# Kernel optimization log

Hardware: AMD Instinct MI355X
Metric: run time of the kernel (lower is better)

Reference implementation:

```python
import jax, jax.numpy as jnp
import numpy as np

B, C, H, W = 4096, 1, 64, 64
NCLASS = 10
ALPHA = 1.0
EPS = 1e-8  # torch CosineSimilarity eps


def setup_inputs() -> dict:
    key = jax.random.key(0)
    k1, k2, k3 = jax.random.split(key, 3)
    outputs = jax.random.normal(k1, (B, NCLASS), dtype=jnp.float32)
    grad = jax.random.normal(k2, (B, C, H, W), dtype=jnp.float32)
    y = jax.random.randint(k3, (B,), 0, NCLASS)
    return {"outputs": outputs, "grad": grad, "y": y}


def reference(outputs, grad, y):
    b = grad.shape[0]
    # per-sample min-max normalization over all of (C,H,W)
    flat = grad.reshape(b, -1)                      # [B, C*H*W]
    gmax = flat.max(axis=1, keepdims=True)
    gmin = flat.min(axis=1, keepdims=True)
    ngrad = (flat - gmin) / (gmax - gmin)           # [B, D]

    # batched pairwise cosine similarity: normalize + matmul
    norms = jnp.linalg.norm(ngrad, axis=1, keepdims=True)
    vn = ngrad / jnp.maximum(norms, EPS)
    sim = vn @ vn.T                                 # [B, B]

    # pairs (i<j) with the same predicted class (argmax(softmax(o)) == argmax(o))
    pred = jnp.argmax(outputs, axis=1)
    same = pred[:, None] == pred[None, :]
    upper = jnp.triu(jnp.ones((b, b), dtype=bool), k=1)
    mask = same & upper
    xloss = jnp.sum(jnp.where(mask, 1.0 - sim, 0.0)) / b

    # cross-entropy
    logp = jax.nn.log_softmax(outputs, axis=1)
    celoss = -jnp.take_along_axis(logp, y[:, None], axis=1).sum() / b
    return celoss + ALPHA * xloss
```

## Files before the change

kernel.cpp:

```cpp
#include <hip/hip_runtime.h>
#include <math.h>

constexpr int Dn = 4096;
constexpr int Bn = 4096;
constexpr int NCLS = 10;
constexpr int CH = 4;
constexpr int MAXCH = Bn / CH + NCLS;

constexpr int OFF_CUR  = 0;
constexpr int OFF_CE   = 10;
constexpr int OFF_XS   = 11;
constexpr int OFF_DONE = 12;
constexpr int OFF_ORD  = 16;
constexpr int OFF_P    = 41024;

__global__ __launch_bounds__(256) void pass0_ce_order(
    const float* __restrict__ outputs, const int* __restrict__ y,
    float* __restrict__ ws)
{
    const int t = threadIdx.x;
    const int i = blockIdx.x * 256 + t;
    const int w = t >> 6, lane = t & 63;
    int* wsi = (int*)ws;

    __shared__ int hist[NCLS];
    __shared__ int lbase[NCLS];
    __shared__ float sce[4];
    if (t < NCLS) hist[t] = 0;
    __syncthreads();

    const float* o = outputs + (size_t)i * NCLS;
    float m = o[0]; int am = 0;
    #pragma unroll
    for (int k = 1; k < NCLS; ++k) { float ok = o[k]; if (ok > m) { m = ok; am = k; } }
    float se = 0.f;
    #pragma unroll
    for (int k = 0; k < NCLS; ++k) se += expf(o[k] - m);
    float ce = m + logf(se) - o[y[i]];

    int rank = atomicAdd(&hist[am], 1);

    #pragma unroll
    for (int off = 32; off; off >>= 1) ce += __shfl_down(ce, off, 64);
    if (lane == 0) sce[w] = ce;
    __syncthreads();

    if (t < NCLS) lbase[t] = atomicAdd(&wsi[OFF_CUR + t], hist[t]);
    if (t == 0) atomicAdd(&ws[OFF_CE], sce[0] + sce[1] + sce[2] + sce[3]);
    __syncthreads();

    wsi[OFF_ORD + am * Bn + lbase[am] + rank] = i;
}

__global__ __launch_bounds__(256) void pass12_fused(
    const float* __restrict__ grad, float* __restrict__ ws)
{
    const int* wsi = (const int*)ws;
    const int t = threadIdx.x, w = t >> 6, lane = t & 63;

    int c = -1, s0 = 0, cnt = 0;
    {
        int b = (int)blockIdx.x, acc = 0;
        #pragma unroll
        for (int k = 0; k < NCLS; ++k) {
            int n = wsi[OFF_CUR + k];
            int nch = (n + CH - 1) / CH;
            if (c < 0 && b < acc + nch) { c = k; s0 = (b - acc) * CH; cnt = n; }
            acc += nch;
        }
    }
    if (c < 0) return;
    const int m = min(CH, cnt - s0);

    float4 v[16];
    if (w < m) {
        const int idx = wsi[OFF_ORD + c * Bn + s0 + w];
        const float4* row = (const float4*)grad + (size_t)idx * (Dn / 4);
        #pragma unroll
        for (int k = 0; k < 16; ++k) v[k] = row[k * 64 + lane];

        float mn = fminf(fminf(v[0].x, v[0].y), fminf(v[0].z, v[0].w));
        #pragma unroll
        for (int k = 1; k < 16; ++k)
            mn = fminf(mn, fminf(fminf(v[k].x, v[k].y), fminf(v[k].z, v[k].w)));
        #pragma unroll
        for (int off = 1; off < 64; off <<= 1)
            mn = fminf(mn, __shfl_xor(mn, off, 64));

        float ss = 0.f;
        #pragma unroll
        for (int k = 0; k < 16; ++k) {
            float dx = v[k].x - mn, dy = v[k].y - mn;
            float dz = v[k].z - mn, dw = v[k].w - mn;
            ss += dx * dx + dy * dy + dz * dz + dw * dw;
        }
        #pragma unroll
        for (int off = 1; off < 64; off <<= 1)
            ss += __shfl_xor(ss, off, 64);

        const float a = 1.0f / sqrtf(ss);
        const float b = -mn * a;
        #pragma unroll
        for (int k = 0; k < 16; ++k) {
            v[k].x = fmaf(v[k].x, a, b);
            v[k].y = fmaf(v[k].y, a, b);
            v[k].z = fmaf(v[k].z, a, b);
            v[k].w = fmaf(v[k].w, a, b);
        }
    } else {
        #pragma unroll
        for (int k = 0; k < 16; ++k) v[k] = make_float4(0.f, 0.f, 0.f, 0.f);
    }

    __shared__ float4 buf0[1024];
    __shared__ float4 buf1[1024];
    if (w == 2) {
        #pragma unroll
        for (int k = 0; k < 16; ++k) buf0[k * 64 + lane] = v[k];
    }
    if (w == 3) {
        #pragma unroll
        for (int k = 0; k < 16; ++k) buf1[k * 64 + lane] = v[k];
    }
    __syncthreads();
    if (w == 0) {
        #pragma unroll
        for (int k = 0; k < 16; ++k) {
            float4 u = buf0[k * 64 + lane];
            v[k].x += u.x; v[k].y += u.y; v[k].z += u.z; v[k].w += u.w;
        }
    }
    if (w == 1) {
        #pragma unroll
        for (int k = 0; k < 16; ++k) {
            float4 u = buf1[k * 64 + lane];
            v[k].x += u.x; v[k].y += u.y; v[k].z += u.z; v[k].w += u.w;
            buf1[k * 64 + lane] = v[k];
        }
    }
    __syncthreads();
    if (w == 0) {
        float4* Pc = (float4*)(ws + OFF_P) + (size_t)blockIdx.x * (Dn / 4);
        #pragma unroll
        for (int k = 0; k < 16; ++k) {
            float4 u = buf1[k * 64 + lane];
            v[k].x += u.x; v[k].y += u.y; v[k].z += u.z; v[k].w += u.w;
            Pc[k * 64 + lane] = v[k];
        }
    }
}

__global__ __launch_bounds__(256) void pass34_final(
    float* __restrict__ ws, float* __restrict__ out)
{
    const int t = threadIdx.x;
    const int idx = blockIdx.x * 256 + t;
    const int c = idx >> 12;
    const int j = idx & (Dn - 1);
    const int w = t >> 6, lane = t & 63;
    const int* wsi = (const int*)ws;

    int cs = 0, ce2 = 0;
    {
        int acc = 0;
        #pragma unroll
        for (int k = 0; k < NCLS; ++k) {
            int nch = (wsi[OFF_CUR + k] + CH - 1) / CH;
            if (k == c) { cs = acc; ce2 = acc + nch; }
            acc += nch;
        }
    }

    const float* P = ws + OFF_P;
    float s = 0.f;
    int ch = cs;
    for (; ch + 4 <= ce2; ch += 4)
        s += P[(size_t)(ch + 0) * Dn + j] + P[(size_t)(ch + 1) * Dn + j]
           + P[(size_t)(ch + 2) * Dn + j] + P[(size_t)(ch + 3) * Dn + j];
    for (; ch < ce2; ++ch) s += P[(size_t)ch * Dn + j];
    float p = s * s;

    #pragma unroll
    for (int off = 32; off; off >>= 1) p += __shfl_down(p, off, 64);
    __shared__ float sr[4];
    if (lane == 0) sr[w] = p;
    __syncthreads();
    if (t == 0) {
        atomicAdd(&ws[OFF_XS], sr[0] + sr[1] + sr[2] + sr[3]);
        __threadfence();
        int ticket = atomicAdd(&((int*)ws)[OFF_DONE], 1);
        if (ticket == (NCLS * Dn / 256) - 1) {
            float xs = atomicAdd(&ws[OFF_XS], 0.0f);
            const int* n = wsi + OFF_CUR;
            double n2 = 0.0;
            #pragma unroll
            for (int k = 0; k < NCLS; ++k) { double nc = (double)n[k]; n2 += nc * nc; }
            double xloss = (n2 - (double)xs) / (2.0 * (double)Bn);
            double celoss = (double)ws[OFF_CE] / (double)Bn;
            out[0] = (float)(celoss + xloss);
        }
    }
}

extern "C" void kernel_launch(void* const* d_in, const int* in_sizes, int n_in,
                              void* d_out, int out_size, void* d_ws, size_t ws_size,
                              hipStream_t stream)
{
    const float* outputs = (const float*)d_in[0];
    const float* grad    = (const float*)d_in[1];
    const int*   y       = (const int*)d_in[2];
    float* ws  = (float*)d_ws;
    float* out = (float*)d_out;

    hipMemsetAsync(d_ws, 0, 64, stream);
    pass0_ce_order<<<Bn / 256, 256, 0, stream>>>(outputs, y, ws);
    pass12_fused<<<MAXCH, 256, 0, stream>>>(grad, ws);
    pass34_final<<<NCLS * Dn / 256, 256, 0, stream>>>(ws, out);
}
```

Baseline: 118.4 us.

## Drop workspace memset by writing per-block class counts and CE partials

```diff
diff --git a/kernel.cpp b/kernel.cpp
--- a/kernel.cpp
+++ b/kernel.cpp
@@ -5,26 +5,27 @@
 constexpr int Bn = 4096;
 constexpr int NCLS = 10;
 constexpr int CH = 4;
+constexpr int NBLK0 = Bn / 256;
 constexpr int MAXCH = Bn / CH + NCLS;
 
-constexpr int OFF_CUR  = 0;
-constexpr int OFF_CE   = 10;
-constexpr int OFF_XS   = 11;
-constexpr int OFF_DONE = 12;
-constexpr int OFF_ORD  = 16;
-constexpr int OFF_P    = 41024;
+constexpr int OFF_CEB  = 0;
+constexpr int OFF_CNT  = 16;
+constexpr int OFF_XS   = 176;
+constexpr int OFF_DONE = 177;
+constexpr int OFF_ORDB = 192;
+constexpr int OFF_P    = 41216;
 
 __global__ __launch_bounds__(256) void pass0_ce_order(
     const float* __restrict__ outputs, const int* __restrict__ y,
     float* __restrict__ ws)
 {
     const int t = threadIdx.x;
-    const int i = blockIdx.x * 256 + t;
+    const int b = blockIdx.x;
+    const int i = b * 256 + t;
     const int w = t >> 6, lane = t & 63;
     int* wsi = (int*)ws;
 
     __shared__ int hist[NCLS];
-    __shared__ int lbase[NCLS];
     __shared__ float sce[4];
     if (t < NCLS) hist[t] = 0;
     __syncthreads();
@@ -39,17 +40,16 @@
     float ce = m + logf(se) - o[y[i]];
 
     int rank = atomicAdd(&hist[am], 1);
+    wsi[OFF_ORDB + (b * NCLS + am) * 256 + rank] = i;
 
     #pragma unroll
     for (int off = 32; off; off >>= 1) ce += __shfl_down(ce, off, 64);
     if (lane == 0) sce[w] = ce;
     __syncthreads();
 
-    if (t < NCLS) lbase[t] = atomicAdd(&wsi[OFF_CUR + t], hist[t]);
-    if (t == 0) atomicAdd(&ws[OFF_CE], sce[0] + sce[1] + sce[2] + sce[3]);
-    __syncthreads();
-
-    wsi[OFF_ORD + am * Bn + lbase[am] + rank] = i;
+    if (t < NCLS) wsi[OFF_CNT + b * NCLS + t] = hist[t];
+    if (t == 0) ws[OFF_CEB + b] = sce[0] + sce[1] + sce[2] + sce[3];
+    if (b == 0 && t == 32) { ws[OFF_XS] = 0.f; wsi[OFF_DONE] = 0; }
 }
 
 __global__ __launch_bounds__(256) void pass12_fused(
@@ -58,14 +58,26 @@
     const int* wsi = (const int*)ws;
     const int t = threadIdx.x, w = t >> 6, lane = t & 63;
 
+    __shared__ int lcnt[NBLK0 * NCLS];
+    __shared__ int tot[NCLS];
+    if (t < NBLK0 * NCLS) lcnt[t] = wsi[OFF_CNT + t];
+    __syncthreads();
+    if (t < NCLS) {
+        int s = 0;
+        #pragma unroll
+        for (int bb = 0; bb < NBLK0; ++bb) s += lcnt[bb * NCLS + t];
+        tot[t] = s;
+    }
+    __syncthreads();
+
     int c = -1, s0 = 0, cnt = 0;
     {
-        int b = (int)blockIdx.x, acc = 0;
+        int bidx = (int)blockIdx.x, acc = 0;
         #pragma unroll
         for (int k = 0; k < NCLS; ++k) {
-            int n = wsi[OFF_CUR + k];
+            int n = tot[k];
             int nch = (n + CH - 1) / CH;
-            if (c < 0 && b < acc + nch) { c = k; s0 = (b - acc) * CH; cnt = n; }
+            if (c < 0 && bidx < acc + nch) { c = k; s0 = (bidx - acc) * CH; cnt = n; }
             acc += nch;
         }
     }
@@ -74,7 +86,18 @@
 
     float4 v[16];
     if (w < m) {
-        const int idx = wsi[OFF_ORD + c * Bn + s0 + w];
+        int idx;
+        {
+            const int r = s0 + w;
+            int pref = 0, src = 0, loc = 0;
+            #pragma unroll
+            for (int bb = 0; bb < NBLK0; ++bb) {
+                int n = lcnt[bb * NCLS + c];
+                if (r >= pref && r < pref + n) { src = bb; loc = r - pref; }
+                pref += n;
+            }
+            idx = wsi[OFF_ORDB + (src * NCLS + c) * 256 + loc];
+        }
         const float4* row = (const float4*)grad + (size_t)idx * (Dn / 4);
         #pragma unroll
         for (int k = 0; k < 16; ++k) v[k] = row[k * 64 + lane];
@@ -112,30 +135,31 @@
         for (int k = 0; k < 16; ++k) v[k] = make_float4(0.f, 0.f, 0.f, 0.f);
     }
 
-    __shared__ float4 buf0[1024];
-    __shared__ float4 buf1[1024];
+    __shared__ float4 buf[1024];
+    if (w == 1) {
+        #pragma unroll
+        for (int k = 0; k < 16; ++k) buf[k * 64 + lane] = v[k];
+    }
+    __syncthreads();
+    if (w == 0) {
+        #pragma unroll
+        for (int k = 0; k < 16; ++k) {
+            float4 u = buf[k * 64 + lane];
+            v[k].x += u.x; v[k].y += u.y; v[k].z += u.z; v[k].w += u.w;
+        }
+    }
+    __syncthreads();
+    if (w == 3) {
+        #pragma unroll
+        for (int k = 0; k < 16; ++k) buf[k * 64 + lane] = v[k];
+    }
+    __syncthreads();
     if (w == 2) {
         #pragma unroll
-        for (int k = 0; k < 16; ++k) buf0[k * 64 + lane] = v[k];
-    }
-    if (w == 3) {
-        #pragma unroll
-        for (int k = 0; k < 16; ++k) buf1[k * 64 + lane] = v[k];
-    }
-    __syncthreads();
-    if (w == 0) {
-        #pragma unroll
-        for (int k = 0; k < 16; ++k) {
-            float4 u = buf0[k * 64 + lane];
+        for (int k = 0; k < 16; ++k) {
+            float4 u = buf[k * 64 + lane];
             v[k].x += u.x; v[k].y += u.y; v[k].z += u.z; v[k].w += u.w;
-        }
-    }
-    if (w == 1) {
-        #pragma unroll
-        for (int k = 0; k < 16; ++k) {
-            float4 u = buf1[k * 64 + lane];
-            v[k].x += u.x; v[k].y += u.y; v[k].z += u.z; v[k].w += u.w;
-            buf1[k * 64 + lane] = v[k];
+            buf[k * 64 + lane] = v[k];
         }
     }
     __syncthreads();
@@ -143,7 +167,7 @@
         float4* Pc = (float4*)(ws + OFF_P) + (size_t)blockIdx.x * (Dn / 4);
         #pragma unroll
         for (int k = 0; k < 16; ++k) {
-            float4 u = buf1[k * 64 + lane];
+            float4 u = buf[k * 64 + lane];
             v[k].x += u.x; v[k].y += u.y; v[k].z += u.z; v[k].w += u.w;
             Pc[k * 64 + lane] = v[k];
         }
@@ -160,12 +184,21 @@
     const int w = t >> 6, lane = t & 63;
     const int* wsi = (const int*)ws;
 
+    __shared__ int tot[NCLS];
+    if (t < NCLS) {
+        int s = 0;
+        #pragma unroll
+        for (int bb = 0; bb < NBLK0; ++bb) s += wsi[OFF_CNT + bb * NCLS + t];
+        tot[t] = s;
+    }
+    __syncthreads();
+
     int cs = 0, ce2 = 0;
     {
         int acc = 0;
         #pragma unroll
         for (int k = 0; k < NCLS; ++k) {
-            int nch = (wsi[OFF_CUR + k] + CH - 1) / CH;
+            int nch = (tot[k] + CH - 1) / CH;
             if (k == c) { cs = acc; ce2 = acc + nch; }
             acc += nch;
         }
@@ -191,13 +224,14 @@
         int ticket = atomicAdd(&((int*)ws)[OFF_DONE], 1);
         if (ticket == (NCLS * Dn / 256) - 1) {
             float xs = atomicAdd(&ws[OFF_XS], 0.0f);
-            const int* n = wsi + OFF_CUR;
             double n2 = 0.0;
             #pragma unroll
-            for (int k = 0; k < NCLS; ++k) { double nc = (double)n[k]; n2 += nc * nc; }
+            for (int k = 0; k < NCLS; ++k) { double nc = (double)tot[k]; n2 += nc * nc; }
+            double cesum = 0.0;
+            #pragma unroll
+            for (int k = 0; k < NBLK0; ++k) cesum += (double)ws[OFF_CEB + k];
             double xloss = (n2 - (double)xs) / (2.0 * (double)Bn);
-            double celoss = (double)ws[OFF_CE] / (double)Bn;
-            out[0] = (float)(celoss + xloss);
+            out[0] = (float)(cesum / (double)Bn + xloss);
         }
     }
 }
@@ -212,8 +246,7 @@
     float* ws  = (float*)d_ws;
     float* out = (float*)d_out;
 
-    hipMemsetAsync(d_ws, 0, 64, stream);
-    pass0_ce_order<<<Bn / 256, 256, 0, stream>>>(outputs, y, ws);
+    pass0_ce_order<<<NBLK0, 256, 0, stream>>>(outputs, y, ws);
     pass12_fused<<<MAXCH, 256, 0, stream>>>(grad, ws);
     pass34_final<<<NCLS * Dn / 256, 256, 0, stream>>>(ws, out);
 }
```

Result: no change. 117.4 us (-0.8%).
